# Performance work log

Hardware: AMD Instinct MI355X
Metric: run time of the kernel (lower is better)

The kernel has to match this reference:

```python
import jax, jax.numpy as jnp
import numpy as np

HIDDEN = 1024

def setup_inputs() -> dict:
    key = jax.random.key(0)
    ks = jax.random.split(key, 7)
    scale = 1.0 / np.sqrt(HIDDEN)
    x = jax.random.normal(ks[0], (4, 2048, HIDDEN), dtype=jnp.float32)
    Wq = jax.random.uniform(ks[1], (HIDDEN, HIDDEN), jnp.float32, -scale, scale)
    bq = jax.random.uniform(ks[2], (HIDDEN,), jnp.float32, -scale, scale)
    Wk = jax.random.uniform(ks[3], (HIDDEN, HIDDEN), jnp.float32, -scale, scale)
    bk = jax.random.uniform(ks[4], (HIDDEN,), jnp.float32, -scale, scale)
    Wv = jax.random.uniform(ks[5], (HIDDEN, HIDDEN), jnp.float32, -scale, scale)
    bv = jax.random.uniform(ks[6], (HIDDEN,), jnp.float32, -scale, scale)
    return {"x": x, "Wq": Wq, "bq": bq, "Wk": Wk, "bk": bk, "Wv": Wv, "bv": bv}

def reference(x, Wq, bq, Wk, bk, Wv, bv):
    # x: [n, t, e]; weights stored as [in, out] so y = x @ W + b
    q = jnp.einsum('nte,ef->ntf', x, Wq) + bq
    k = jnp.einsum('nte,ef->ntf', x, Wk) + bk
    v = jnp.einsum('nte,ef->ntf', x, Wv) + bv
    scores = jnp.einsum('nqe,nke->nqk', q, k)  # unscaled, as in the original
    alpha = jax.nn.softmax(scores, axis=2)
    return jnp.einsum('nqk,nke->nqe', alpha, v)
```

## Files before the change

### kernel.cpp

```cpp
#include <hip/hip_runtime.h>
#include <stdint.h>

typedef __attribute__((ext_vector_type(4))) float f32x4;
typedef __attribute__((ext_vector_type(8))) _Float16 f16x8;
typedef __attribute__((ext_vector_type(8))) unsigned short u16x8;

#define HIDDEN 1024
#define SEQ 2048
#define NB 4

__device__ inline unsigned short f2h_bits(float f) {
    _Float16 h = (_Float16)f;
    return __builtin_bit_cast(unsigned short, h);
}
__device__ inline float h2f(unsigned short u) {
    return (float)__builtin_bit_cast(_Float16, u);
}

__device__ inline void gload16(const void* g, void* l) {
    __builtin_amdgcn_global_load_lds(
        (const __attribute__((address_space(1))) unsigned int*)g,
        (__attribute__((address_space(3))) unsigned int*)l,
        16, 0, 0);
}

template<int N> __device__ inline void waitvm() {
    if constexpr (N == 0) asm volatile("s_waitcnt vmcnt(0)" ::: "memory");
    else if constexpr (N == 3) asm volatile("s_waitcnt vmcnt(3)" ::: "memory");
    else if constexpr (N == 4) asm volatile("s_waitcnt vmcnt(4)" ::: "memory");
    else if constexpr (N == 6) asm volatile("s_waitcnt vmcnt(6)" ::: "memory");
    else if constexpr (N == 8) asm volatile("s_waitcnt vmcnt(8)" ::: "memory");
    else static_assert(N == 0, "bad vmcnt");
}
template<int N> __device__ inline void waitlgkm() {
    if constexpr (N == 0) asm volatile("s_waitcnt lgkmcnt(0)" ::: "memory");
    else if constexpr (N == 2) asm volatile("s_waitcnt lgkmcnt(2)" ::: "memory");
    else if constexpr (N == 4) asm volatile("s_waitcnt lgkmcnt(4)" ::: "memory");
    else static_assert(N == 0, "bad lgkmcnt");
}

template<int BM, int BN, int WM, int WN, int BIAS_MODE, bool OUT_F16, int MINW>
__global__ __launch_bounds__(WM * WN * 64, MINW) void gemm8p(
    const unsigned short* __restrict__ A, int lda,
    const unsigned short* __restrict__ Bt, int ldb,
    const float* __restrict__ bias,
    void* __restrict__ Cptr, int ldc, int K,
    long long aBatch, long long bBatch, long long cBatch)
{
    constexpr int THREADS = WM * WN * 64;
    constexpr int MR = BM / (WM * 16);
    constexpr int NRW = BN / (WN * 16);
    constexpr int MH = MR / 2;
    constexpr int LA = 4 * BM / THREADS;
    constexpr int LB = 4 * BN / THREADS;
    constexpr int LP = LA + LB;
    constexpr int ASLICE = BM * 32;
    constexpr int BSLICE = BN * 32;
    constexpr int BOFF = 4 * ASLICE;

    extern __shared__ unsigned short lds[];

    const int tid = threadIdx.x, lane = tid & 63, wave = tid >> 6;
    const int wr = wave / WN, wc = wave % WN;
    const int fr = lane & 15, fq = lane >> 4;

    const int gx = gridDim.x, gy = gridDim.y;
    const int nwg = gx * gy * gridDim.z;
    const int id = (blockIdx.z * gy + blockIdx.y) * gx + blockIdx.x;
    const int id2 = (id & 7) * (nwg >> 3) + (id >> 3);
    const int bx = id2 % gx;
    const int by = (id2 / gx) % gy;
    const long long bz = id2 / (gx * gy);

    const unsigned short* Ab = A + bz * aBatch + (long long)(by * BM) * lda;
    const unsigned short* Bb = Bt + bz * bBatch + (long long)(bx * BN) * ldb;

    const unsigned short* sA[LA]; int dA[LA];
    #pragma unroll
    for (int i = 0; i < LA; ++i) {
        int c = i * THREADS + tid; int r = c >> 2; int ls = (c & 3) ^ ((r >> 1) & 3);
        sA[i] = Ab + (long long)r * lda + ls * 8;
        dA[i] = (i * THREADS + wave * 64) * 16;
    }
    const unsigned short* sB[LB]; int dB[LB];
    #pragma unroll
    for (int i = 0; i < LB; ++i) {
        int c = i * THREADS + tid; int r = c >> 2; int ls = (c & 3) ^ ((r >> 1) & 3);
        sB[i] = Bb + (long long)r * ldb + ls * 8;
        dB[i] = (i * THREADS + wave * 64) * 16;
    }

    auto stage = [&](int q) {
        int slot = q & 3;
        int kof = q * 32;
        #pragma unroll
        for (int i = 0; i < LA; ++i)
            gload16(sA[i] + kof, (char*)lds + slot * (ASLICE * 2) + dA[i]);
        #pragma unroll
        for (int i = 0; i < LB; ++i)
            gload16(sB[i] + kof, (char*)lds + (BOFF + slot * BSLICE) * 2 + dB[i]);
    };

    const int NPAIR = K / 32;
    stage(0); stage(1); stage(2);

    f32x4 acc[MR][NRW] = {};

    for (int p = 0; p < NPAIR; ++p) {
        if (p == NPAIR - 1) waitvm<0>();
        else if (p == NPAIR - 2) waitvm<LP>();
        else waitvm<2 * LP>();
        __builtin_amdgcn_s_barrier();
        __builtin_amdgcn_sched_barrier(0);

        const int slot = p & 3;
        const unsigned short* as = lds + slot * ASLICE;
        const unsigned short* bs = lds + BOFF + slot * BSLICE;

        f16x8 af[MR], bf[NRW];
        #pragma unroll
        for (int n = 0; n < NRW; ++n) {
            int r = wc * (BN / WN) + n * 16 + fr;
            int es = fq ^ ((r >> 1) & 3);
            bf[n] = *(const f16x8*)&bs[r * 32 + es * 8];
        }
        #pragma unroll
        for (int m = 0; m < MH; ++m) {
            int r = wr * (BM / WM) + m * 16 + fr;
            int es = fq ^ ((r >> 1) & 3);
            af[m] = *(const f16x8*)&as[r * 32 + es * 8];
        }
        if (p + 3 < NPAIR) stage(p + 3);
        #pragma unroll
        for (int m = MH; m < MR; ++m) {
            int r = wr * (BM / WM) + m * 16 + fr;
            int es = fq ^ ((r >> 1) & 3);
            af[m] = *(const f16x8*)&as[r * 32 + es * 8];
        }

        waitlgkm<MR - MH>();
        __builtin_amdgcn_sched_barrier(0);
        __builtin_amdgcn_s_setprio(1);
        #pragma unroll
        for (int m = 0; m < MH; ++m)
            #pragma unroll
            for (int n = 0; n < NRW; ++n)
                acc[m][n] = __builtin_amdgcn_mfma_f32_16x16x32_f16(af[m], bf[n], acc[m][n], 0, 0, 0);
        __builtin_amdgcn_s_setprio(0);
        __builtin_amdgcn_sched_barrier(0);
        waitlgkm<0>();
        __builtin_amdgcn_sched_barrier(0);
        __builtin_amdgcn_s_setprio(1);
        #pragma unroll
        for (int m = MH; m < MR; ++m)
            #pragma unroll
            for (int n = 0; n < NRW; ++n)
                acc[m][n] = __builtin_amdgcn_mfma_f32_16x16x32_f16(af[m], bf[n], acc[m][n], 0, 0, 0);
        __builtin_amdgcn_s_setprio(0);
    }

    const int row0 = by * BM + wr * (BM / WM);
    const int col0 = bx * BN + wc * (BN / WN);
    #pragma unroll
    for (int m = 0; m < MR; ++m)
        #pragma unroll
        for (int n = 0; n < NRW; ++n)
            #pragma unroll
            for (int i = 0; i < 4; ++i) {
                int r = row0 + m * 16 + fq * 4 + i;
                int c = col0 + n * 16 + fr;
                float v = acc[m][n][i];
                if constexpr (BIAS_MODE == 1) v += bias[c];
                if constexpr (BIAS_MODE == 2) v += bias[r];
                if constexpr (OUT_F16)
                    ((unsigned short*)Cptr + bz * cBatch)[(long long)r * ldc + c] = f2h_bits(v);
                else
                    ((float*)Cptr + bz * cBatch)[(long long)r * ldc + c] = v;
            }
}

__global__ __launch_bounds__(256) void cvt_f32_f16(const float* __restrict__ in,
                                                   unsigned short* __restrict__ out, int n8)
{
    int i = blockIdx.x * blockDim.x + threadIdx.x;
    if (i >= n8) return;
    const float4* p = (const float4*)in + (long long)i * 2;
    float4 a = p[0], b = p[1];
    ushort4 o0, o1;
    o0.x = f2h_bits(a.x); o0.y = f2h_bits(a.y); o0.z = f2h_bits(a.z); o0.w = f2h_bits(a.w);
    o1.x = f2h_bits(b.x); o1.y = f2h_bits(b.y); o1.z = f2h_bits(b.z); o1.w = f2h_bits(b.w);
    ushort4* o = (ushort4*)out + (long long)i * 2;
    o[0] = o0; o[1] = o1;
}

__global__ void transpose_cvt(const float* __restrict__ in, unsigned short* __restrict__ out,
                              int R, int C)
{
    __shared__ unsigned short t[32][33];
    const int bx = blockIdx.x * 32;
    const int by = blockIdx.y * 32;
    const int xT = threadIdx.x, yT = threadIdx.y;
    #pragma unroll
    for (int i = 0; i < 32; i += 8)
        t[yT + i][xT] = f2h_bits(in[(long long)(by + yT + i) * C + bx + xT]);
    __syncthreads();
    #pragma unroll
    for (int i = 0; i < 32; i += 8)
        out[(long long)(bx + yT + i) * R + by + xT] = t[xT][yT + i];
}

__global__ void concat_bias2(const float* __restrict__ bq, const float* __restrict__ bk,
                             float* __restrict__ cb)
{
    int i = threadIdx.x;
    cb[i] = bq[i];
    cb[HIDDEN + i] = bk[i];
}

__global__ __launch_bounds__(256) void softmax_h(unsigned short* __restrict__ S)
{
    const int tid = threadIdx.x;
    unsigned short* row = S + (long long)blockIdx.x * SEQ;
    u16x8 hv = *(const u16x8*)&row[tid * 8];
    float vv[8];
    #pragma unroll
    for (int j = 0; j < 8; ++j) vv[j] = h2f(hv[j]);

    float mx = vv[0];
    #pragma unroll
    for (int j = 1; j < 8; ++j) mx = fmaxf(mx, vv[j]);
    #pragma unroll
    for (int o = 32; o > 0; o >>= 1) mx = fmaxf(mx, __shfl_xor(mx, o));
    __shared__ float redm[4], reds[4];
    if ((tid & 63) == 0) redm[tid >> 6] = mx;
    __syncthreads();
    mx = fmaxf(fmaxf(redm[0], redm[1]), fmaxf(redm[2], redm[3]));

    float ev[8], sum = 0.f;
    #pragma unroll
    for (int j = 0; j < 8; ++j) { ev[j] = __expf(vv[j] - mx); sum += ev[j]; }
    #pragma unroll
    for (int o = 32; o > 0; o >>= 1) sum += __shfl_xor(sum, o);
    if ((tid & 63) == 0) reds[tid >> 6] = sum;
    __syncthreads();
    sum = reds[0] + reds[1] + reds[2] + reds[3];
    float inv = 1.0f / sum;

    u16x8 ov;
    #pragma unroll
    for (int j = 0; j < 8; ++j) ov[j] = f2h_bits(ev[j] * inv);
    *(u16x8*)&row[tid * 8] = ov;
}

extern "C" void kernel_launch(void* const* d_in, const int* in_sizes, int n_in,
                              void* d_out, int out_size, void* d_ws, size_t ws_size,
                              hipStream_t stream)
{
    (void)in_sizes; (void)n_in; (void)out_size; (void)ws_size;
    const float* x  = (const float*)d_in[0];
    const float* Wq = (const float*)d_in[1];
    const float* bq = (const float*)d_in[2];
    const float* Wk = (const float*)d_in[3];
    const float* bk = (const float*)d_in[4];
    const float* Wv = (const float*)d_in[5];
    const float* bv = (const float*)d_in[6];
    float* out = (float*)d_out;

    (void)hipFuncSetAttribute(reinterpret_cast<const void*>(&gemm8p<256, 256, 2, 4, 1, true, 2>),
                              hipFuncAttributeMaxDynamicSharedMemorySize, 131072);
    (void)hipFuncSetAttribute(reinterpret_cast<const void*>(&gemm8p<256, 256, 2, 4, 0, true, 2>),
                              hipFuncAttributeMaxDynamicSharedMemorySize, 131072);
    (void)hipFuncSetAttribute(reinterpret_cast<const void*>(&gemm8p<128, 256, 2, 4, 2, true, 2>),
                              hipFuncAttributeMaxDynamicSharedMemorySize, 98304);
    (void)hipFuncSetAttribute(reinterpret_cast<const void*>(&gemm8p<256, 128, 2, 4, 0, false, 2>),
                              hipFuncAttributeMaxDynamicSharedMemorySize, 98304);

    char* ws = (char*)d_ws;
    const long long MTOT = (long long)NB * SEQ;

    unsigned short* qk = (unsigned short*)ws;
    unsigned short* vt = (unsigned short*)(ws + (size_t)MTOT * 2048 * 2);
    char* sreg = ws + (size_t)MTOT * 2048 * 2 + (size_t)HIDDEN * MTOT * 2;
    unsigned short* wt = (unsigned short*)sreg;
    float* cb = (float*)(sreg + (size_t)3 * HIDDEN * HIDDEN * 2);
    unsigned short* xh = (unsigned short*)(sreg + (size_t)3 * HIDDEN * HIDDEN * 2 + 8192);
    unsigned short* S = (unsigned short*)sreg;

    {
        int n8 = (int)(MTOT * HIDDEN / 8);
        cvt_f32_f16<<<dim3((n8 + 255) / 256), 256, 0, stream>>>(x, xh, n8);
    }
    dim3 tb(32, 8), tg(HIDDEN / 32, HIDDEN / 32);
    transpose_cvt<<<tg, tb, 0, stream>>>(Wq, wt,                       HIDDEN, HIDDEN);
    transpose_cvt<<<tg, tb, 0, stream>>>(Wk, wt +     HIDDEN * HIDDEN, HIDDEN, HIDDEN);
    transpose_cvt<<<tg, tb, 0, stream>>>(Wv, wt + 2 * HIDDEN * HIDDEN, HIDDEN, HIDDEN);
    concat_bias2<<<1, 1024, 0, stream>>>(bq, bk, cb);

    gemm8p<256, 256, 2, 4, 1, true, 2><<<dim3(2048 / 256, (unsigned)(MTOT / 256), 1), 512, 131072, stream>>>(
        xh, HIDDEN, wt, HIDDEN, cb, qk, 2048, HIDDEN, 0, 0, 0);

    gemm8p<128, 256, 2, 4, 2, true, 2><<<dim3((unsigned)(MTOT / 256), HIDDEN / 128, 1), 512, 98304, stream>>>(
        wt + 2 * HIDDEN * HIDDEN, HIDDEN, xh, HIDDEN, bv, vt, (int)MTOT, HIDDEN, 0, 0, 0);

    gemm8p<256, 256, 2, 4, 0, true, 2><<<dim3(SEQ / 256, SEQ / 256, NB), 512, 131072, stream>>>(
        qk, 2048, qk + HIDDEN, 2048, nullptr, S, SEQ, HIDDEN,
        (long long)SEQ * 2048, (long long)SEQ * 2048, (long long)SEQ * SEQ);

    softmax_h<<<dim3(NB * SEQ), 256, 0, stream>>>(S);

    gemm8p<256, 128, 2, 4, 0, false, 2><<<dim3(HIDDEN / 128, SEQ / 256, NB), 512, 98304, stream>>>(
        S, SEQ, vt, (int)MTOT, nullptr, out, HIDDEN, SEQ,
        (long long)SEQ * SEQ, (long long)SEQ, (long long)SEQ * HIDDEN);
}
```

Before: 173.2 us.

## Split GEMM stage loads into A/B halves interleaved with MFMA phases

Restructures the GEMM main loop into a ping-pong style schedule: the A and B tile prefetches are issued separately, each paired with one half of the MFMA work, with extra workgroup barriers between phases. The vmcnt wait moves to the end of the iteration and the prologue waits before the loop. The goal is to spread global-to-LDS traffic and LDS reads across compute phases so memory and MFMA overlap better across waves. It adds more barriers per iteration and full lgkmcnt(0) waits, which may serialize waves.

```diff
diff --git a/kernel.cpp b/kernel.cpp
--- a/kernel.cpp
+++ b/kernel.cpp
@@ -32,12 +32,7 @@
     else if constexpr (N == 8) asm volatile("s_waitcnt vmcnt(8)" ::: "memory");
     else static_assert(N == 0, "bad vmcnt");
 }
-template<int N> __device__ inline void waitlgkm() {
-    if constexpr (N == 0) asm volatile("s_waitcnt lgkmcnt(0)" ::: "memory");
-    else if constexpr (N == 2) asm volatile("s_waitcnt lgkmcnt(2)" ::: "memory");
-    else if constexpr (N == 4) asm volatile("s_waitcnt lgkmcnt(4)" ::: "memory");
-    else static_assert(N == 0, "bad lgkmcnt");
-}
+__device__ inline void waitlgkm0() { asm volatile("s_waitcnt lgkmcnt(0)" ::: "memory"); }
 
 template<int BM, int BN, int WM, int WN, int BIAS_MODE, bool OUT_F16, int MINW>
 __global__ __launch_bounds__(WM * WN * 64, MINW) void gemm8p(
@@ -90,34 +85,32 @@
         dB[i] = (i * THREADS + wave * 64) * 16;
     }
 
-    auto stage = [&](int q) {
-        int slot = q & 3;
-        int kof = q * 32;
+    auto stageA = [&](int q) {
+        int slot = q & 3, kof = q * 32;
         #pragma unroll
         for (int i = 0; i < LA; ++i)
             gload16(sA[i] + kof, (char*)lds + slot * (ASLICE * 2) + dA[i]);
+    };
+    auto stageB = [&](int q) {
+        int slot = q & 3, kof = q * 32;
         #pragma unroll
         for (int i = 0; i < LB; ++i)
             gload16(sB[i] + kof, (char*)lds + (BOFF + slot * BSLICE) * 2 + dB[i]);
     };
 
     const int NPAIR = K / 32;
-    stage(0); stage(1); stage(2);
+    stageA(0); stageB(0); stageA(1); stageB(1); stageA(2); stageB(2);
+    waitvm<2 * LP>();
+    __builtin_amdgcn_s_barrier();
 
     f32x4 acc[MR][NRW] = {};
 
     for (int p = 0; p < NPAIR; ++p) {
-        if (p == NPAIR - 1) waitvm<0>();
-        else if (p == NPAIR - 2) waitvm<LP>();
-        else waitvm<2 * LP>();
-        __builtin_amdgcn_s_barrier();
-        __builtin_amdgcn_sched_barrier(0);
-
         const int slot = p & 3;
         const unsigned short* as = lds + slot * ASLICE;
         const unsigned short* bs = lds + BOFF + slot * BSLICE;
-
         f16x8 af[MR], bf[NRW];
+
         #pragma unroll
         for (int n = 0; n < NRW; ++n) {
             int r = wc * (BN / WN) + n * 16 + fr;
@@ -130,25 +123,28 @@
             int es = fq ^ ((r >> 1) & 3);
             af[m] = *(const f16x8*)&as[r * 32 + es * 8];
         }
-        if (p + 3 < NPAIR) stage(p + 3);
+        if (p + 3 < NPAIR) stageA(p + 3);
+        __builtin_amdgcn_s_barrier();
+        waitlgkm0();
+        __builtin_amdgcn_sched_barrier(0);
+        __builtin_amdgcn_s_setprio(1);
+        #pragma unroll
+        for (int m = 0; m < MH; ++m)
+            #pragma unroll
+            for (int n = 0; n < NRW; ++n)
+                acc[m][n] = __builtin_amdgcn_mfma_f32_16x16x32_f16(af[m], bf[n], acc[m][n], 0, 0, 0);
+        __builtin_amdgcn_s_setprio(0);
+        __builtin_amdgcn_s_barrier();
+
         #pragma unroll
         for (int m = MH; m < MR; ++m) {
             int r = wr * (BM / WM) + m * 16 + fr;
             int es = fq ^ ((r >> 1) & 3);
             af[m] = *(const f16x8*)&as[r * 32 + es * 8];
         }
-
-        waitlgkm<MR - MH>();
-        __builtin_amdgcn_sched_barrier(0);
-        __builtin_amdgcn_s_setprio(1);
-        #pragma unroll
-        for (int m = 0; m < MH; ++m)
-            #pragma unroll
-            for (int n = 0; n < NRW; ++n)
-                acc[m][n] = __builtin_amdgcn_mfma_f32_16x16x32_f16(af[m], bf[n], acc[m][n], 0, 0, 0);
-        __builtin_amdgcn_s_setprio(0);
-        __builtin_amdgcn_sched_barrier(0);
-        waitlgkm<0>();
+        if (p + 3 < NPAIR) stageB(p + 3);
+        __builtin_amdgcn_s_barrier();
+        waitlgkm0();
         __builtin_amdgcn_sched_barrier(0);
         __builtin_amdgcn_s_setprio(1);
         #pragma unroll
@@ -157,6 +153,10 @@
             for (int n = 0; n < NRW; ++n)
                 acc[m][n] = __builtin_amdgcn_mfma_f32_16x16x32_f16(af[m], bf[n], acc[m][n], 0, 0, 0);
         __builtin_amdgcn_s_setprio(0);
+        if (p < NPAIR - 3) waitvm<2 * LP>();
+        else if (p == NPAIR - 3) waitvm<LP>();
+        else if (p == NPAIR - 2) waitvm<0>();
+        __builtin_amdgcn_s_barrier();
     }
 
     const int row0 = by * BM + wr * (BM / WM);
```

Result: slower. 181.3 us (+4.7%).

## Replace templated GEMM with fixed 256x128 four-wave tile and triple-buffered pipeline

Applied to the files above, without the earlier changes.

All four GEMMs now use one kernel with a 256x128 block tile, 4 waves of 128x64 each, and a 3-slot LDS ring instead of 4 slots with 8 waves. Each wave holds twice as many accumulators, so more MFMA work is done per LDS fragment load, and LDS use drops to 72KB so more blocks can fit per CU. The cost is a shallower prefetch depth (two stages ahead instead of three), higher register pressure per thread, and smaller tiles for the QK and QKV GEMMs, which means more blocks and more global reads.

```diff
diff --git a/kernel.cpp b/kernel.cpp
--- a/kernel.cpp
+++ b/kernel.cpp
@@ -26,42 +26,37 @@
 
 template<int N> __device__ inline void waitvm() {
     if constexpr (N == 0) asm volatile("s_waitcnt vmcnt(0)" ::: "memory");
-    else if constexpr (N == 3) asm volatile("s_waitcnt vmcnt(3)" ::: "memory");
-    else if constexpr (N == 4) asm volatile("s_waitcnt vmcnt(4)" ::: "memory");
     else if constexpr (N == 6) asm volatile("s_waitcnt vmcnt(6)" ::: "memory");
-    else if constexpr (N == 8) asm volatile("s_waitcnt vmcnt(8)" ::: "memory");
     else static_assert(N == 0, "bad vmcnt");
 }
 template<int N> __device__ inline void waitlgkm() {
     if constexpr (N == 0) asm volatile("s_waitcnt lgkmcnt(0)" ::: "memory");
-    else if constexpr (N == 2) asm volatile("s_waitcnt lgkmcnt(2)" ::: "memory");
     else if constexpr (N == 4) asm volatile("s_waitcnt lgkmcnt(4)" ::: "memory");
     else static_assert(N == 0, "bad lgkmcnt");
 }
 
-template<int BM, int BN, int WM, int WN, int BIAS_MODE, bool OUT_F16, int MINW>
-__global__ __launch_bounds__(WM * WN * 64, MINW) void gemm8p(
+template<int BIAS_MODE, bool OUT_F16>
+__global__ __launch_bounds__(256, 2) void gemm2b(
     const unsigned short* __restrict__ A, int lda,
     const unsigned short* __restrict__ Bt, int ldb,
     const float* __restrict__ bias,
     void* __restrict__ Cptr, int ldc, int K,
     long long aBatch, long long bBatch, long long cBatch)
 {
-    constexpr int THREADS = WM * WN * 64;
-    constexpr int MR = BM / (WM * 16);
-    constexpr int NRW = BN / (WN * 16);
-    constexpr int MH = MR / 2;
+    constexpr int BM = 256, BN = 128;
+    constexpr int THREADS = 256;
+    constexpr int MR = 8, NRW = 4, MH = 4;
     constexpr int LA = 4 * BM / THREADS;
     constexpr int LB = 4 * BN / THREADS;
     constexpr int LP = LA + LB;
     constexpr int ASLICE = BM * 32;
     constexpr int BSLICE = BN * 32;
-    constexpr int BOFF = 4 * ASLICE;
+    constexpr int BOFF = 3 * ASLICE;
 
     extern __shared__ unsigned short lds[];
 
     const int tid = threadIdx.x, lane = tid & 63, wave = tid >> 6;
-    const int wr = wave / WN, wc = wave % WN;
+    const int wr = wave >> 1, wc = wave & 1;
     const int fr = lane & 15, fq = lane >> 4;
 
     const int gx = gridDim.x, gy = gridDim.y;
@@ -91,8 +86,7 @@
     }
 
     auto stage = [&](int q) {
-        int slot = q & 3;
-        int kof = q * 32;
+        int slot = q % 3, kof = q * 32;
         #pragma unroll
         for (int i = 0; i < LA; ++i)
             gload16(sA[i] + kof, (char*)lds + slot * (ASLICE * 2) + dA[i]);
@@ -102,43 +96,42 @@
     };
 
     const int NPAIR = K / 32;
-    stage(0); stage(1); stage(2);
+    stage(0); stage(1);
 
     f32x4 acc[MR][NRW] = {};
 
     for (int p = 0; p < NPAIR; ++p) {
         if (p == NPAIR - 1) waitvm<0>();
-        else if (p == NPAIR - 2) waitvm<LP>();
-        else waitvm<2 * LP>();
+        else waitvm<LP>();
         __builtin_amdgcn_s_barrier();
         __builtin_amdgcn_sched_barrier(0);
 
-        const int slot = p & 3;
+        const int slot = p % 3;
         const unsigned short* as = lds + slot * ASLICE;
         const unsigned short* bs = lds + BOFF + slot * BSLICE;
 
         f16x8 af[MR], bf[NRW];
         #pragma unroll
         for (int n = 0; n < NRW; ++n) {
-            int r = wc * (BN / WN) + n * 16 + fr;
+            int r = wc * 64 + n * 16 + fr;
             int es = fq ^ ((r >> 1) & 3);
             bf[n] = *(const f16x8*)&bs[r * 32 + es * 8];
         }
         #pragma unroll
         for (int m = 0; m < MH; ++m) {
-            int r = wr * (BM / WM) + m * 16 + fr;
+            int r = wr * 128 + m * 16 + fr;
             int es = fq ^ ((r >> 1) & 3);
             af[m] = *(const f16x8*)&as[r * 32 + es * 8];
         }
-        if (p + 3 < NPAIR) stage(p + 3);
+        if (p + 2 < NPAIR) stage(p + 2);
         #pragma unroll
         for (int m = MH; m < MR; ++m) {
-            int r = wr * (BM / WM) + m * 16 + fr;
+            int r = wr * 128 + m * 16 + fr;
             int es = fq ^ ((r >> 1) & 3);
             af[m] = *(const f16x8*)&as[r * 32 + es * 8];
         }
 
-        waitlgkm<MR - MH>();
+        waitlgkm<4>();
         __builtin_amdgcn_sched_barrier(0);
         __builtin_amdgcn_s_setprio(1);
         #pragma unroll
@@ -159,8 +152,8 @@
         __builtin_amdgcn_s_setprio(0);
     }
 
-    const int row0 = by * BM + wr * (BM / WM);
-    const int col0 = bx * BN + wc * (BN / WN);
+    const int row0 = by * BM + wr * 128;
+    const int col0 = bx * BN + wc * 64;
     #pragma unroll
     for (int m = 0; m < MR; ++m)
         #pragma unroll
@@ -266,14 +259,14 @@
     const float* bv = (const float*)d_in[6];
     float* out = (float*)d_out;
 
-    (void)hipFuncSetAttribute(reinterpret_cast<const void*>(&gemm8p<256, 256, 2, 4, 1, true, 2>),
-                              hipFuncAttributeMaxDynamicSharedMemorySize, 131072);
-    (void)hipFuncSetAttribute(reinterpret_cast<const void*>(&gemm8p<256, 256, 2, 4, 0, true, 2>),
-                              hipFuncAttributeMaxDynamicSharedMemorySize, 131072);
-    (void)hipFuncSetAttribute(reinterpret_cast<const void*>(&gemm8p<128, 256, 2, 4, 2, true, 2>),
-                              hipFuncAttributeMaxDynamicSharedMemorySize, 98304);
-    (void)hipFuncSetAttribute(reinterpret_cast<const void*>(&gemm8p<256, 128, 2, 4, 0, false, 2>),
-                              hipFuncAttributeMaxDynamicSharedMemorySize, 98304);
+    (void)hipFuncSetAttribute(reinterpret_cast<const void*>(&gemm2b<1, true>),
+                              hipFuncAttributeMaxDynamicSharedMemorySize, 73728);
+    (void)hipFuncSetAttribute(reinterpret_cast<const void*>(&gemm2b<2, true>),
+                              hipFuncAttributeMaxDynamicSharedMemorySize, 73728);
+    (void)hipFuncSetAttribute(reinterpret_cast<const void*>(&gemm2b<0, true>),
+                              hipFuncAttributeMaxDynamicSharedMemorySize, 73728);
+    (void)hipFuncSetAttribute(reinterpret_cast<const void*>(&gemm2b<0, false>),
+                              hipFuncAttributeMaxDynamicSharedMemorySize, 73728);
 
     char* ws = (char*)d_ws;
     const long long MTOT = (long long)NB * SEQ;
@@ -296,19 +289,19 @@
     transpose_cvt<<<tg, tb, 0, stream>>>(Wv, wt + 2 * HIDDEN * HIDDEN, HIDDEN, HIDDEN);
     concat_bias2<<<1, 1024, 0, stream>>>(bq, bk, cb);
 
-    gemm8p<256, 256, 2, 4, 1, true, 2><<<dim3(2048 / 256, (unsigned)(MTOT / 256), 1), 512, 131072, stream>>>(
+    gemm2b<1, true><<<dim3(2048 / 128, (unsigned)(MTOT / 256), 1), 256, 73728, stream>>>(
         xh, HIDDEN, wt, HIDDEN, cb, qk, 2048, HIDDEN, 0, 0, 0);
 
-    gemm8p<128, 256, 2, 4, 2, true, 2><<<dim3((unsigned)(MTOT / 256), HIDDEN / 128, 1), 512, 98304, stream>>>(
+    gemm2b<2, true><<<dim3((unsigned)(MTOT / 128), HIDDEN / 256, 1), 256, 73728, stream>>>(
         wt + 2 * HIDDEN * HIDDEN, HIDDEN, xh, HIDDEN, bv, vt, (int)MTOT, HIDDEN, 0, 0, 0);
 
-    gemm8p<256, 256, 2, 4, 0, true, 2><<<dim3(SEQ / 256, SEQ / 256, NB), 512, 131072, stream>>>(
+    gemm2b<0, true><<<dim3(SEQ / 128, SEQ / 256, NB), 256, 73728, stream>>>(
         qk, 2048, qk + HIDDEN, 2048, nullptr, S, SEQ, HIDDEN,
         (long long)SEQ * 2048, (long long)SEQ * 2048, (long long)SEQ * SEQ);
 
     softmax_h<<<dim3(NB * SEQ), 256, 0, stream>>>(S);
 
-    gemm8p<256, 128, 2, 4, 0, false, 2><<<dim3(HIDDEN / 128, SEQ / 256, NB), 512, 98304, stream>>>(
+    gemm2b<0, false><<<dim3(HIDDEN / 128, SEQ / 256, NB), 256, 73728, stream>>>(
         S, SEQ, vt, (int)MTOT, nullptr, out, HIDDEN, SEQ,
         (long long)SEQ * SEQ, (long long)SEQ, (long long)SEQ * HIDDEN);
 }
```

After: 182.2 us. 5.2% more time.
